# Performance work log

Hardware: AMD Instinct MI355X
Metric: run time of the kernel (lower is better)

The kernel has to match this reference:

```python
import jax, jax.numpy as jnp
import numpy as np

D_MODEL = 2048
N_HEADS = 16
D_HEAD = 128
ROPE_THETA = 10000.0


def _rope(x, offset):
    # x: [B, H, S, D]; half-rotation RoPE with position offset
    B, H, S, D = x.shape
    inv_freq = 1.0 / (ROPE_THETA ** (jnp.arange(0, D, 2, dtype=jnp.float32) / D))  # [D/2]
    pos = (offset + jnp.arange(S, dtype=jnp.float32))                              # [S]
    ang = pos[:, None] * inv_freq[None, :]                                         # [S, D/2]
    cos = jnp.cos(ang).astype(x.dtype)
    sin = jnp.sin(ang).astype(x.dtype)
    x1, x2 = x[..., : D // 2], x[..., D // 2 :]
    return jnp.concatenate([x1 * cos - x2 * sin, x2 * cos + x1 * sin], axis=-1)


def setup_inputs() -> dict:
    key = jax.random.key(0)
    ks = jax.random.split(key, 5)
    B, Sq, Skv = 4, 1024, 1024
    x = jax.random.normal(ks[0], (B, Sq, D_MODEL), dtype=jnp.float32)
    cache_k = jax.random.normal(ks[1], (B, N_HEADS, Skv, D_HEAD), dtype=jnp.float32)
    cache_v = jax.random.normal(ks[2], (B, N_HEADS, Skv, D_HEAD), dtype=jnp.float32)
    w_qkv = jax.random.normal(ks[3], (D_MODEL, 3 * D_MODEL), dtype=jnp.float32) * (D_MODEL ** -0.5)
    w_o = jax.random.normal(ks[4], (D_MODEL, D_MODEL), dtype=jnp.float32) * (D_MODEL ** -0.5)
    return {"x": x, "cache_k": cache_k, "cache_v": cache_v, "w_qkv": w_qkv, "w_o": w_o}


def reference(x, cache_k, cache_v, w_qkv, w_o):
    B, S, _ = x.shape
    offset = cache_k.shape[2]
    # fused QKV projection: [B, S, 3*d_model] -> [B, H, S, 3*d_head]
    qkv = jnp.einsum("bsd,de->bse", x, w_qkv)
    qkv = qkv.reshape(B, S, N_HEADS, 3 * D_HEAD).transpose(0, 2, 1, 3)
    q, k, v = jnp.split(qkv, 3, axis=-1)
    q = _rope(q, offset)
    k = _rope(k, offset)
    # KV-cache concat along sequence dim
    k = jnp.concatenate([cache_k, k], axis=2)  # [B, H, Skv+S, D]
    v = jnp.concatenate([cache_v, v], axis=2)
    # SDPA (no mask, matching mask=None path)
    scale = D_HEAD ** -0.5
    scores = jnp.einsum("bhqd,bhkd->bhqk", q, k) * scale
    attn = jax.nn.softmax(scores, axis=-1)
    out = jnp.einsum("bhqk,bhkd->bhqd", attn, v)           # [B, H, S, D]
    out = out.transpose(0, 2, 1, 3).reshape(B, S, D_MODEL)
    return jnp.einsum("bsd,de->bse", out, w_o)
```

## Files before the change

kernel.cpp:

```cpp
#include <hip/hip_runtime.h>


typedef __bf16 bf16x8 __attribute__((ext_vector_type(8)));
typedef float f32x4 __attribute__((ext_vector_type(4)));
typedef unsigned short u16x8 __attribute__((ext_vector_type(8)));
typedef unsigned short u16x4 __attribute__((ext_vector_type(4)));

__device__ __forceinline__ float b2f(unsigned short u) {
  return __builtin_bit_cast(float, (unsigned int)u << 16);
}
__device__ __forceinline__ unsigned short f2b(float f) {
  unsigned int x = __builtin_bit_cast(unsigned int, f);
  x += 0x7fffu + ((x >> 16) & 1u);
  return (unsigned short)(x >> 16);
}
__device__ __forceinline__ unsigned int cvt_pk_bf16(float lo, float hi) {
  unsigned int r;
  asm("v_cvt_pk_bf16_f32 %0, %1, %2" : "=v"(r) : "v"(lo), "v"(hi));
  return r;
}
__device__ __forceinline__ void gload_lds16(const void* g, void* l) {
  __builtin_amdgcn_global_load_lds(
      (__attribute__((address_space(1))) void*)(g),
      (__attribute__((address_space(3))) void*)(l), 16, 0, 0);
}
__device__ __forceinline__ void barrier_nodrain() {
  asm volatile("" ::: "memory");
  __builtin_amdgcn_s_barrier();
  asm volatile("" ::: "memory");
}

__global__ __launch_bounds__(256) void prep_fused(
    const float* __restrict__ x, const float* __restrict__ ck,
    const float* __restrict__ wqkv, const float* __restrict__ wo,
    unsigned short* __restrict__ xb, unsigned short* __restrict__ Kf,
    unsigned short* __restrict__ wqT, unsigned short* __restrict__ woT,
    float* __restrict__ cs, float* __restrict__ sn) {
  __shared__ float tile[32][33];
  int id = blockIdx.x;
  if (id < 4096) {
    size_t i = ((size_t)id * 256 + threadIdx.x) * 8;
    float4 a = *(const float4*)(x + i);
    float4 b = *(const float4*)(x + i + 4);
    u16x8 v;
    v[0] = f2b(a.x); v[1] = f2b(a.y); v[2] = f2b(a.z); v[3] = f2b(a.w);
    v[4] = f2b(b.x); v[5] = f2b(b.y); v[6] = f2b(b.z); v[7] = f2b(b.w);
    *(u16x8*)(xb + i) = v;
  } else if (id < 20480) {
    const float* in;  unsigned short* out;  int R, C, idx;
    if (id < 16384) { in = wqkv; out = wqT; R = 2048; C = 6144; idx = id - 4096; }
    else            { in = wo;   out = woT; R = 2048; C = 2048; idx = id - 16384; }
    int nc = C >> 5;
    int c0 = (idx % nc) * 32, r0 = (idx / nc) * 32;
    int tx = threadIdx.x & 31, ty = threadIdx.x >> 5;
#pragma unroll
    for (int j = 0; j < 4; ++j)
      tile[ty + j * 8][tx] = in[(size_t)(r0 + ty + j * 8) * C + c0 + tx];
    __syncthreads();
#pragma unroll
    for (int j = 0; j < 4; ++j)
      out[(size_t)(c0 + ty + j * 8) * R + r0 + tx] = f2b(tile[tx][ty + j * 8]);
  } else if (id < 28672) {
    size_t idx = ((size_t)(id - 20480) * 256 + threadIdx.x) * 4;
    size_t bh = idx >> 17, rem = idx & 131071;
    float4 a = *(const float4*)(ck + idx);
    u16x4 v;
    v[0] = f2b(a.x); v[1] = f2b(a.y); v[2] = f2b(a.z); v[3] = f2b(a.w);
    *(u16x4*)(Kf + bh * 262144 + rem) = v;
  } else {
    int idx = (id - 28672) * 256 + threadIdx.x;
    int s = idx >> 6, i = idx & 63;
    float inv = exp2f(-(float)i * (13.287712379549449f / 64.0f));
    float ang = (float)(1024 + s) * inv;
    cs[idx] = cosf(ang);
    sn[idx] = sinf(ang);
  }
}

__global__ __launch_bounds__(256) void post_fused(
    const unsigned short* __restrict__ qkv, const float* __restrict__ cs,
    const float* __restrict__ sn, const float* __restrict__ cv,
    unsigned short* __restrict__ Qb, unsigned short* __restrict__ Kf,
    unsigned short* __restrict__ Vt) {
  __shared__ float tile[32][33];
  int id = blockIdx.x;
  if (id < 4096) {
    int row = id;
    int b = row >> 10, s = row & 1023;
#pragma unroll
    for (int it = 0; it < 4; ++it) {
      int item = it * 256 + threadIdx.x;
      int h = item >> 6, i = item & 63;
      const unsigned short* base = qkv + (size_t)row * 6144 + h * 384;
      float q1 = b2f(base[i]),       q2 = b2f(base[64 + i]);
      float k1 = b2f(base[128 + i]), k2 = b2f(base[192 + i]);
      float c = cs[s * 64 + i], sv = sn[s * 64 + i];
      const float scale = 0.12751738f;
      size_t bh = (size_t)(b * 16 + h);
      unsigned short* qd = Qb + (bh * 1024 + s) * 128;
      qd[i]      = f2b((q1 * c - q2 * sv) * scale);
      qd[64 + i] = f2b((q2 * c + q1 * sv) * scale);
      unsigned short* kd = Kf + (bh * 2048 + 1024 + s) * 128;
      kd[i]      = f2b(k1 * c - k2 * sv);
      kd[64 + i] = f2b(k2 * c + k1 * sv);
    }
  } else {
    int idx = id - 4096;
    int bhid = idx >> 8;
    int rem = idx & 255;
    int d0 = (rem >> 6) * 32, s0 = (rem & 63) * 32;
    int tx = threadIdx.x & 31, ty = threadIdx.x >> 5;
    int b = bhid >> 4, h = bhid & 15;
#pragma unroll
    for (int j = 0; j < 4; ++j) {
      int s = s0 + ty + j * 8, d = d0 + tx;
      float v;
      if (s < 1024) v = cv[((size_t)bhid * 1024 + s) * 128 + d];
      else v = b2f(qkv[((size_t)b * 1024 + (s - 1024)) * 6144 + h * 384 + 256 + d]);
      tile[ty + j * 8][tx] = v;
    }
    __syncthreads();
#pragma unroll
    for (int j = 0; j < 4; ++j) {
      int d = d0 + ty + j * 8, s = s0 + tx;
      Vt[((size_t)bhid * 128 + d) * 2048 + s] = f2b(tile[tx][ty + j * 8]);
    }
  }
}

template <int M, int N, int K, bool OUT_BF16>
__global__ __launch_bounds__(512, 4) void gemm_ring(
    const unsigned short* __restrict__ A, const unsigned short* __restrict__ B,
    void* __restrict__ Cout) {
  __shared__ __align__(16) char lds[3 * 24576];
  constexpr int NT = N / 128;
  constexpr int Kt = K / 32;
  int bid = blockIdx.x;
  int tm = bid / NT, tn = bid % NT;
  int tid = threadIdx.x;
  int lane = tid & 63, wave = tid >> 6;
  int wr = (wave >> 1) * 64, wc = (wave & 1) * 64;
  int l15 = lane & 15, g = lane >> 4;
  int rcol = (g * 16) ^ (((l15 >> 1) & 3) << 4);

  int p = tid * 16;
  int srcCol = (p & 63) ^ (((p >> 7) & 3) << 4);
  const unsigned short* aSrc0 = A + (size_t)(tm * 256 + (p >> 6)) * K + (srcCol >> 1);
  const unsigned short* aSrc1 = aSrc0 + (size_t)128 * K;
  const unsigned short* bSrc  = B + (size_t)(tn * 128 + (p >> 6)) * K + (srcCol >> 1);

  f32x4 acc[4][4] = {};

  auto stage = [&](int s) {
    char* base = (char*)lds + s * 24576;
    gload_lds16(aSrc0, base + p);
    gload_lds16(aSrc1, base + 8192 + p);
    gload_lds16(bSrc,  base + 16384 + p);
    aSrc0 += 32; aSrc1 += 32; bSrc += 32;
  };

  stage(0);
  stage(1);
  asm volatile("s_waitcnt vmcnt(3)" ::: "memory");

  int slot = 0, sNext = 2;
  for (int t = 0; t < Kt; ++t) {
    barrier_nodrain();
    if (t + 2 < Kt) {
      stage(sNext);
      sNext = (sNext == 2) ? 0 : sNext + 1;
      asm volatile("s_waitcnt vmcnt(3)" ::: "memory");
    } else {
      asm volatile("s_waitcnt vmcnt(0)" ::: "memory");
    }
    const char* As_ = (const char*)lds + slot * 24576;
    const char* Bs_ = As_ + 16384;
    bf16x8 af[4], bfr[4];
#pragma unroll
    for (int m = 0; m < 4; ++m)
      af[m] = *(const bf16x8*)(As_ + (wr + m * 16 + l15) * 64 + rcol);
#pragma unroll
    for (int n = 0; n < 4; ++n)
      bfr[n] = *(const bf16x8*)(Bs_ + (wc + n * 16 + l15) * 64 + rcol);
    __builtin_amdgcn_s_setprio(1);
#pragma unroll
    for (int m = 0; m < 4; ++m)
#pragma unroll
      for (int n = 0; n < 4; ++n)
        acc[m][n] = __builtin_amdgcn_mfma_f32_16x16x32_bf16(af[m], bfr[n], acc[m][n], 0, 0, 0);
    __builtin_amdgcn_s_setprio(0);
    slot = (slot == 2) ? 0 : slot + 1;
  }

#pragma unroll
  for (int m = 0; m < 4; ++m) {
    int row0 = tm * 256 + wr + m * 16 + g * 4;
#pragma unroll
    for (int n = 0; n < 4; ++n) {
      int col = tn * 128 + wc + n * 16 + l15;
#pragma unroll
      for (int r = 0; r < 4; ++r) {
        size_t off = (size_t)(row0 + r) * N + col;
        if constexpr (OUT_BF16) ((unsigned short*)Cout)[off] = f2b(acc[m][n][r]);
        else ((float*)Cout)[off] = acc[m][n][r];
      }
    }
  }
}

__global__ __launch_bounds__(256, 2) void attn_kernel(
    const unsigned short* __restrict__ Qb,
    const unsigned short* __restrict__ Kf,
    const unsigned short* __restrict__ Vt,
    unsigned short* __restrict__ Out) {
  __shared__ __align__(16) unsigned short Ks[2][64 * 128];
  __shared__ __align__(16) unsigned short Vs[2][64 * 128];
  __shared__ __align__(16) char PsRaw[4 * 2 * 2048];

  int raw = blockIdx.x;
  int sb = (raw & 7) * 64 + (raw >> 3);
  int bh = sb >> 3, qt = sb & 7;
  int tid = threadIdx.x, lane = tid & 63, wave = tid >> 6;
  int l15 = lane & 15, g = lane >> 4;
  int swz = (l15 & 7) << 4;

  int qrow0 = qt * 128 + wave * 32;
  bf16x8 qf0[4], qf1[4];
  const unsigned short* qp0 = Qb + ((size_t)(bh * 1024 + qrow0 + l15)) * 128;
#pragma unroll
  for (int kk = 0; kk < 4; ++kk) {
    qf0[kk] = *(const bf16x8*)(qp0 + kk * 32 + g * 8);
    qf1[kk] = *(const bf16x8*)(qp0 + 16 * 128 + kk * 32 + g * 8);
  }

  u16x8 ou;
#pragma unroll
  for (int j = 0; j < 8; ++j) ou[j] = 0x3F80;
  bf16x8 ones = __builtin_bit_cast(bf16x8, ou);

  const unsigned short* Kbase = Kf + (size_t)bh * 2048 * 128;
  const unsigned short* Vbase = Vt + (size_t)bh * 128 * 2048;
  const unsigned short* kptr[4];
  const unsigned short* vptr[4];
  char* kdst0[4];
  char* vdst0[4];
#pragma unroll
  for (int is = 0; is < 4; ++is) {
    int p = tid * 16 + is * 4096;
    int lgk = p ^ (((p >> 8) & 7) << 4);
    kptr[is] = Kbase + (size_t)(lgk >> 8) * 128 + ((lgk & 255) >> 1);
    kdst0[is] = (char*)Ks + is * 4096 + (tid & 192) * 16;
    int lgv = p ^ (((p >> 7) & 7) << 4);
    vptr[is] = Vbase + (size_t)(lgv >> 7) * 2048 + ((lgv & 127) >> 1);
    vdst0[is] = (char*)Vs + is * 4096 + (tid & 192) * 16;
  }
  char* ps0 = PsRaw + wave * 4096 + l15 * 128;
  char* ps1 = ps0 + 2048;

  auto stage = [&](int buf) {
#pragma unroll
    for (int is = 0; is < 4; ++is) {
      gload_lds16(kptr[is], kdst0[is] + buf * 16384);  kptr[is] += 64 * 128;
      gload_lds16(vptr[is], vdst0[is] + buf * 16384);  vptr[is] += 64;
    }
  };

  float mrun0 = -1e30f, mrun1 = -1e30f;
  f32x4 acc0[8] = {}, acc1[8] = {};
  f32x4 accl0 = {}, accl1 = {};

  auto softmax_pack = [&](f32x4* st, float& mrun, f32x4* accp, f32x4& accl,
                          char* ps) {
    float m0 = fmaxf(fmaxf(st[0][0], st[0][1]), st[0][2]);
    float m1 = fmaxf(fmaxf(st[0][3], st[1][0]), st[1][1]);
    float m2 = fmaxf(fmaxf(st[1][2], st[1][3]), st[2][0]);
    float m3 = fmaxf(fmaxf(st[2][1], st[2][2]), st[2][3]);
    float m4 = fmaxf(fmaxf(st[3][0], st[3][1]), st[3][2]);
    float pmax = fmaxf(fmaxf(fmaxf(m0, m1), fmaxf(m2, m3)), fmaxf(m4, st[3][3]));
    pmax = fmaxf(pmax, __shfl_xor(pmax, 16));
    pmax = fmaxf(pmax, __shfl_xor(pmax, 32));
    if (!__all(pmax - mrun <= 8.0f)) {
      float mnew = fmaxf(mrun, pmax);
      float corr = exp2f(mrun - mnew);
      accl *= corr;
#pragma unroll
      for (int mt = 0; mt < 8; ++mt) accp[mt] *= corr;
      mrun = mnew;
    }
#pragma unroll
    for (int t = 0; t < 4; ++t) {
      float p0 = exp2f(st[t][0] - mrun);
      float p1 = exp2f(st[t][1] - mrun);
      float p2 = exp2f(st[t][2] - mrun);
      float p3 = exp2f(st[t][3] - mrun);
      uint2 w;
      w.x = cvt_pk_bf16(p0, p1);
      w.y = cvt_pk_bf16(p2, p3);
      *(uint2*)(ps + ((t * 32 + g * 8) ^ swz)) = w;
    }
  };

  stage(0);
  for (int it = 0; it < 32; ++it) {
    int cur = it & 1;
    barrier_nodrain();
    if (it + 1 < 32) {
      stage(cur ^ 1);
      asm volatile("s_waitcnt vmcnt(8)" ::: "memory");
    } else {
      asm volatile("s_waitcnt vmcnt(0)" ::: "memory");
    }
    barrier_nodrain();
    const char* ksA = (const char*)Ks + cur * 16384 + l15 * 256;
    const char* vsA = (const char*)Vs + cur * 16384 + l15 * 128;

    f32x4 st0[4] = {}, st1[4] = {};
#pragma unroll
    for (int kk = 0; kk < 4; ++kk) {
#pragma unroll
      for (int t = 0; t < 4; ++t) {
        bf16x8 a = *(const bf16x8*)(ksA + t * 4096 + ((kk * 64 + g * 16) ^ swz));
        st0[t] = __builtin_amdgcn_mfma_f32_16x16x32_bf16(a, qf0[kk], st0[t], 0, 0, 0);
        st1[t] = __builtin_amdgcn_mfma_f32_16x16x32_bf16(a, qf1[kk], st1[t], 0, 0, 0);
      }
    }

    softmax_pack(st0, mrun0, acc0, accl0, ps0);
    softmax_pack(st1, mrun1, acc1, accl1, ps1);

#pragma unroll
    for (int k2 = 0; k2 < 2; ++k2) {
      bf16x8 p0 = *(const bf16x8*)(ps0 + ((k2 * 64 + g * 16) ^ swz));
      bf16x8 p1 = *(const bf16x8*)(ps1 + ((k2 * 64 + g * 16) ^ swz));
      accl0 = __builtin_amdgcn_mfma_f32_16x16x32_bf16(ones, p0, accl0, 0, 0, 0);
      accl1 = __builtin_amdgcn_mfma_f32_16x16x32_bf16(ones, p1, accl1, 0, 0, 0);
#pragma unroll
      for (int mt = 0; mt < 8; ++mt) {
        bf16x8 a = *(const bf16x8*)(vsA + mt * 2048 + ((k2 * 64 + g * 16) ^ swz));
        acc0[mt] = __builtin_amdgcn_mfma_f32_16x16x32_bf16(a, p0, acc0[mt], 0, 0, 0);
        acc1[mt] = __builtin_amdgcn_mfma_f32_16x16x32_bf16(a, p1, acc1[mt], 0, 0, 0);
      }
    }
  }

  float inv0 = 1.f / accl0[0];
  float inv1 = 1.f / accl1[0];
  int b = bh >> 4, h = bh & 15;
  int sq = qt * 128 + wave * 32 + l15;
  unsigned short* orow0 = Out + ((size_t)(b * 1024 + sq) * 16 + h) * 128;
  unsigned short* orow1 = orow0 + (size_t)16 * 2048;
#pragma unroll
  for (int mt = 0; mt < 8; ++mt) {
    uint2 w0, w1;
    w0.x = cvt_pk_bf16(acc0[mt][0] * inv0, acc0[mt][1] * inv0);
    w0.y = cvt_pk_bf16(acc0[mt][2] * inv0, acc0[mt][3] * inv0);
    w1.x = cvt_pk_bf16(acc1[mt][0] * inv1, acc1[mt][1] * inv1);
    w1.y = cvt_pk_bf16(acc1[mt][2] * inv1, acc1[mt][3] * inv1);
    *(uint2*)(orow0 + mt * 16 + g * 4) = w0;
    *(uint2*)(orow1 + mt * 16 + g * 4) = w1;
  }
}

extern "C" void kernel_launch(void* const* d_in, const int* in_sizes, int n_in,
                              void* d_out, int out_size, void* d_ws, size_t ws_size,
                              hipStream_t stream) {
  const float* x       = (const float*)d_in[0];
  const float* cache_k = (const float*)d_in[1];
  const float* cache_v = (const float*)d_in[2];
  const float* w_qkv   = (const float*)d_in[3];
  const float* w_o     = (const float*)d_in[4];
  float* out = (float*)d_out;

  char* W = (char*)d_ws;
  constexpr size_t O_TRIG = 0;
  constexpr size_t O_XB   = 524288;
  constexpr size_t O_WQT  = O_XB  + 16777216;
  constexpr size_t O_WOT  = O_WQT + 25165824;
  constexpr size_t O_QKV  = O_WOT + 8388608;
  constexpr size_t O_QB   = O_QKV + 50331648;
  constexpr size_t O_KF   = O_QB  + 16777216;
  constexpr size_t O_VT   = O_KF  + 33554432;
  float* cs_tab = (float*)(W + O_TRIG);
  float* sn_tab = (float*)(W + O_TRIG + 262144);
  unsigned short* xb   = (unsigned short*)(W + O_XB);
  unsigned short* wqT  = (unsigned short*)(W + O_WQT);
  unsigned short* woT  = (unsigned short*)(W + O_WOT);
  unsigned short* qkv  = (unsigned short*)(W + O_QKV);
  unsigned short* qb   = (unsigned short*)(W + O_QB);
  unsigned short* Kf   = (unsigned short*)(W + O_KF);
  unsigned short* Vt   = (unsigned short*)(W + O_VT);
  unsigned short* attn_out = xb;

  prep_fused<<<28928, 256, 0, stream>>>(x, cache_k, w_qkv, w_o,
                                        xb, Kf, wqT, woT, cs_tab, sn_tab);
  gemm_ring<4096, 6144, 2048, true><<<768, 512, 0, stream>>>(xb, wqT, qkv);
  post_fused<<<20480, 256, 0, stream>>>(qkv, cs_tab, sn_tab, cache_v,
                                        qb, Kf, Vt);
  attn_kernel<<<512, 256, 0, stream>>>(qb, Kf, Vt, attn_out);
  gemm_ring<4096, 2048, 2048, false><<<256, 512, 0, stream>>>(attn_out, woT, out);
}
```

Baseline: 319.0 us.

## Fuse RoPE, Q/K/V scatter and V transpose into QKV GEMM epilogue

Removes the post_fused kernel and the intermediate bf16 QKV buffer. The QKV GEMM epilogue now applies RoPE and scaling and writes Q, K and transposed V directly. The wave column mapping is interleaved so each wave holds both RoPE halves of a head tile. The cache_v transpose moves into the prep kernel. This saves a full write and read of the QKV activation and one launch, at the cost of scattered 2-byte stores and table loads in the GEMM epilogue.

```diff
diff --git a/kernel.cpp b/kernel.cpp
--- a/kernel.cpp
+++ b/kernel.cpp
@@ -32,8 +32,9 @@
 
 __global__ __launch_bounds__(256) void prep_fused(
     const float* __restrict__ x, const float* __restrict__ ck,
-    const float* __restrict__ wqkv, const float* __restrict__ wo,
-    unsigned short* __restrict__ xb, unsigned short* __restrict__ Kf,
+    const float* __restrict__ cv, const float* __restrict__ wqkv,
+    const float* __restrict__ wo, unsigned short* __restrict__ xb,
+    unsigned short* __restrict__ Kf, unsigned short* __restrict__ Vt,
     unsigned short* __restrict__ wqT, unsigned short* __restrict__ woT,
     float* __restrict__ cs, float* __restrict__ sn) {
   __shared__ float tile[32][33];
@@ -67,71 +68,36 @@
     u16x4 v;
     v[0] = f2b(a.x); v[1] = f2b(a.y); v[2] = f2b(a.z); v[3] = f2b(a.w);
     *(u16x4*)(Kf + bh * 262144 + rem) = v;
-  } else {
+  } else if (id < 28928) {
     int idx = (id - 28672) * 256 + threadIdx.x;
     int s = idx >> 6, i = idx & 63;
     float inv = exp2f(-(float)i * (13.287712379549449f / 64.0f));
     float ang = (float)(1024 + s) * inv;
     cs[idx] = cosf(ang);
     sn[idx] = sinf(ang);
-  }
-}
-
-__global__ __launch_bounds__(256) void post_fused(
-    const unsigned short* __restrict__ qkv, const float* __restrict__ cs,
-    const float* __restrict__ sn, const float* __restrict__ cv,
-    unsigned short* __restrict__ Qb, unsigned short* __restrict__ Kf,
-    unsigned short* __restrict__ Vt) {
-  __shared__ float tile[32][33];
-  int id = blockIdx.x;
-  if (id < 4096) {
-    int row = id;
-    int b = row >> 10, s = row & 1023;
-#pragma unroll
-    for (int it = 0; it < 4; ++it) {
-      int item = it * 256 + threadIdx.x;
-      int h = item >> 6, i = item & 63;
-      const unsigned short* base = qkv + (size_t)row * 6144 + h * 384;
-      float q1 = b2f(base[i]),       q2 = b2f(base[64 + i]);
-      float k1 = b2f(base[128 + i]), k2 = b2f(base[192 + i]);
-      float c = cs[s * 64 + i], sv = sn[s * 64 + i];
-      const float scale = 0.12751738f;
-      size_t bh = (size_t)(b * 16 + h);
-      unsigned short* qd = Qb + (bh * 1024 + s) * 128;
-      qd[i]      = f2b((q1 * c - q2 * sv) * scale);
-      qd[64 + i] = f2b((q2 * c + q1 * sv) * scale);
-      unsigned short* kd = Kf + (bh * 2048 + 1024 + s) * 128;
-      kd[i]      = f2b(k1 * c - k2 * sv);
-      kd[64 + i] = f2b(k2 * c + k1 * sv);
-    }
   } else {
-    int idx = id - 4096;
-    int bhid = idx >> 8;
-    int rem = idx & 255;
-    int d0 = (rem >> 6) * 32, s0 = (rem & 63) * 32;
+    int idx = id - 28928;
+    int bhid = idx >> 7;
+    int rem = idx & 127;
+    int d0 = (rem >> 5) * 32, s0 = (rem & 31) * 32;
     int tx = threadIdx.x & 31, ty = threadIdx.x >> 5;
-    int b = bhid >> 4, h = bhid & 15;
-#pragma unroll
-    for (int j = 0; j < 4; ++j) {
-      int s = s0 + ty + j * 8, d = d0 + tx;
-      float v;
-      if (s < 1024) v = cv[((size_t)bhid * 1024 + s) * 128 + d];
-      else v = b2f(qkv[((size_t)b * 1024 + (s - 1024)) * 6144 + h * 384 + 256 + d]);
-      tile[ty + j * 8][tx] = v;
-    }
+#pragma unroll
+    for (int j = 0; j < 4; ++j)
+      tile[ty + j * 8][tx] = cv[((size_t)bhid * 1024 + s0 + ty + j * 8) * 128 + d0 + tx];
     __syncthreads();
 #pragma unroll
-    for (int j = 0; j < 4; ++j) {
-      int d = d0 + ty + j * 8, s = s0 + tx;
-      Vt[((size_t)bhid * 128 + d) * 2048 + s] = f2b(tile[tx][ty + j * 8]);
-    }
-  }
-}
-
-template <int M, int N, int K, bool OUT_BF16>
+    for (int j = 0; j < 4; ++j)
+      Vt[((size_t)bhid * 128 + d0 + ty + j * 8) * 2048 + s0 + tx] =
+          f2b(tile[tx][ty + j * 8]);
+  }
+}
+
+template <int M, int N, int K, int MODE>
 __global__ __launch_bounds__(512, 4) void gemm_ring(
     const unsigned short* __restrict__ A, const unsigned short* __restrict__ B,
-    void* __restrict__ Cout) {
+    void* __restrict__ Cout, const float* __restrict__ cs,
+    const float* __restrict__ sn, unsigned short* __restrict__ Qb,
+    unsigned short* __restrict__ Kf, unsigned short* __restrict__ Vt) {
   __shared__ __align__(16) char lds[3 * 24576];
   constexpr int NT = N / 128;
   constexpr int Kt = K / 32;
@@ -139,7 +105,8 @@
   int tm = bid / NT, tn = bid % NT;
   int tid = threadIdx.x;
   int lane = tid & 63, wave = tid >> 6;
-  int wr = (wave >> 1) * 64, wc = (wave & 1) * 64;
+  int wr = (wave >> 1) * 64;
+  int wc1 = wave & 1;
   int l15 = lane & 15, g = lane >> 4;
   int rcol = (g * 16) ^ (((l15 >> 1) & 3) << 4);
 
@@ -181,7 +148,7 @@
       af[m] = *(const bf16x8*)(As_ + (wr + m * 16 + l15) * 64 + rcol);
 #pragma unroll
     for (int n = 0; n < 4; ++n)
-      bfr[n] = *(const bf16x8*)(Bs_ + (wc + n * 16 + l15) * 64 + rcol);
+      bfr[n] = *(const bf16x8*)(Bs_ + (wc1 * 16 + n * 32 + l15) * 64 + rcol);
     __builtin_amdgcn_s_setprio(1);
 #pragma unroll
     for (int m = 0; m < 4; ++m)
@@ -192,17 +159,60 @@
     slot = (slot == 2) ? 0 : slot + 1;
   }
 
-#pragma unroll
-  for (int m = 0; m < 4; ++m) {
-    int row0 = tm * 256 + wr + m * 16 + g * 4;
-#pragma unroll
-    for (int n = 0; n < 4; ++n) {
-      int col = tn * 128 + wc + n * 16 + l15;
-#pragma unroll
-      for (int r = 0; r < 4; ++r) {
-        size_t off = (size_t)(row0 + r) * N + col;
-        if constexpr (OUT_BF16) ((unsigned short*)Cout)[off] = f2b(acc[m][n][r]);
-        else ((float*)Cout)[off] = acc[m][n][r];
+  if constexpr (MODE == 0) {
+#pragma unroll
+    for (int m = 0; m < 4; ++m) {
+      int row0 = tm * 256 + wr + m * 16 + g * 4;
+#pragma unroll
+      for (int n = 0; n < 4; ++n) {
+        int col = tn * 128 + wc1 * 16 + n * 32 + l15;
+#pragma unroll
+        for (int r = 0; r < 4; ++r)
+          ((float*)Cout)[(size_t)(row0 + r) * N + col] = acc[m][n][r];
+      }
+    }
+  } else {
+    int part = tn % 3, h = tn / 3;
+    size_t bh = (size_t)(tm >> 2) * 16 + h;
+    if (part == 2) {
+#pragma unroll
+      for (int m = 0; m < 4; ++m) {
+        int s0 = (tm & 3) * 256 + wr + m * 16 + g * 4;
+#pragma unroll
+        for (int n = 0; n < 4; ++n) {
+          int d = wc1 * 16 + n * 32 + l15;
+          uint2 w;
+          w.x = cvt_pk_bf16(acc[m][n][0], acc[m][n][1]);
+          w.y = cvt_pk_bf16(acc[m][n][2], acc[m][n][3]);
+          *(uint2*)(Vt + (bh * 128 + d) * 2048 + 1024 + s0) = w;
+        }
+      }
+    } else {
+      const float qscale = 0.12751738f;
+#pragma unroll
+      for (int m = 0; m < 4; ++m) {
+        int s0 = (tm & 3) * 256 + wr + m * 16 + g * 4;
+#pragma unroll
+        for (int n = 0; n < 2; ++n) {
+          int i1 = wc1 * 16 + n * 32 + l15;
+#pragma unroll
+          for (int r = 0; r < 4; ++r) {
+            int s = s0 + r;
+            float c = cs[s * 64 + i1], sv = sn[s * 64 + i1];
+            float v1 = acc[m][n][r], v2 = acc[m][n + 2][r];
+            float o1 = v1 * c - v2 * sv;
+            float o2 = v2 * c + v1 * sv;
+            unsigned short* dst;
+            if (part == 0) {
+              o1 *= qscale; o2 *= qscale;
+              dst = Qb + (bh * 1024 + s) * 128;
+            } else {
+              dst = Kf + (bh * 2048 + 1024 + s) * 128;
+            }
+            dst[i1] = f2b(o1);
+            dst[i1 + 64] = f2b(o2);
+          }
+        }
       }
     }
   }
@@ -376,8 +386,7 @@
   constexpr size_t O_XB   = 524288;
   constexpr size_t O_WQT  = O_XB  + 16777216;
   constexpr size_t O_WOT  = O_WQT + 25165824;
-  constexpr size_t O_QKV  = O_WOT + 8388608;
-  constexpr size_t O_QB   = O_QKV + 50331648;
+  constexpr size_t O_QB   = O_WOT + 8388608;
   constexpr size_t O_KF   = O_QB  + 16777216;
   constexpr size_t O_VT   = O_KF  + 33554432;
   float* cs_tab = (float*)(W + O_TRIG);
@@ -385,17 +394,16 @@
   unsigned short* xb   = (unsigned short*)(W + O_XB);
   unsigned short* wqT  = (unsigned short*)(W + O_WQT);
   unsigned short* woT  = (unsigned short*)(W + O_WOT);
-  unsigned short* qkv  = (unsigned short*)(W + O_QKV);
   unsigned short* qb   = (unsigned short*)(W + O_QB);
   unsigned short* Kf   = (unsigned short*)(W + O_KF);
   unsigned short* Vt   = (unsigned short*)(W + O_VT);
   unsigned short* attn_out = xb;
 
-  prep_fused<<<28928, 256, 0, stream>>>(x, cache_k, w_qkv, w_o,
-                                        xb, Kf, wqT, woT, cs_tab, sn_tab);
-  gemm_ring<4096, 6144, 2048, true><<<768, 512, 0, stream>>>(xb, wqT, qkv);
-  post_fused<<<20480, 256, 0, stream>>>(qkv, cs_tab, sn_tab, cache_v,
-                                        qb, Kf, Vt);
+  prep_fused<<<37120, 256, 0, stream>>>(x, cache_k, cache_v, w_qkv, w_o,
+                                        xb, Kf, Vt, wqT, woT, cs_tab, sn_tab);
+  gemm_ring<4096, 6144, 2048, 1><<<768, 512, 0, stream>>>(
+      xb, wqT, nullptr, cs_tab, sn_tab, qb, Kf, Vt);
   attn_kernel<<<512, 256, 0, stream>>>(qb, Kf, Vt, attn_out);
-  gemm_ring<4096, 2048, 2048, false><<<256, 512, 0, stream>>>(attn_out, woT, out);
-}
+  gemm_ring<4096, 2048, 2048, 0><<<256, 512, 0, stream>>>(
+      attn_out, woT, out, nullptr, nullptr, nullptr, nullptr, nullptr);
+}
```

Result: faster. 296.1 us (-7.2%).
